# Kernel tuning notes

Hardware: AMD Instinct MI355X
Metric: run time of the kernel (lower is better)

## Reference

```python
import jax, jax.numpy as jnp
import numpy as np

N, D_IN, D_OUT = 10000, 256, 256


def setup_inputs() -> dict:
    key = jax.random.key(0)
    k1, k2, k3, k4 = jax.random.split(key, 4)
    # xavier_uniform with gain=1.414 (as in the torch module)
    def xavier(k, shape, gain=1.414):
        fan_in, fan_out = shape[0], shape[1]
        bound = gain * np.sqrt(6.0 / (fan_in + fan_out))
        return jax.random.uniform(k, shape, jnp.float32, -bound, bound)
    return {
        "input": jax.random.normal(k1, (N, D_IN), jnp.float32),
        "adj": jax.random.randint(k2, (N, N), 0, 2, jnp.int32),  # binary dense adjacency
        "M": N,
        "W": xavier(k3, (D_IN, D_OUT)),
        "b": jnp.zeros((D_OUT,), jnp.float32),
        "a": xavier(k4, (D_OUT, 1)),
    }


def reference(input, adj, M, W, b, a):
    # h = tanh(X W + b); values used for attention logits
    h = jnp.tanh(input @ W + b)          # [N, F]
    inp = input @ W                      # [N, F] (values to aggregate)
    e = (h @ a)[:, 0]                    # [N] per-node logit
    # original also drops neighbors whose h row sums to exactly 0
    valid = (jnp.sum(h, axis=1) != 0)    # [N]
    mask = (adj[:M] > 0) & valid[None, :]  # [M, N]
    neg = jnp.asarray(-1e30, h.dtype)
    scores = jnp.where(mask, e[None, :], neg)           # [M, N]
    m = jnp.max(scores, axis=1, keepdims=True)
    w = jnp.where(mask, jnp.exp(scores - m), 0.0)       # masked exp
    denom = jnp.sum(w, axis=1, keepdims=True)
    att = w / jnp.maximum(denom, 1e-30)  # rows with no neighbors -> all zeros (matches torch zeros init)
    # dropout is identity in eval mode (training=False)
    return att @ inp                     # [M, F]
```

## Files before the change

kernel.cpp:

```cpp
#include <hip/hip_runtime.h>
#include <hip/hip_bf16.h>
#include <cstdint>
#include <cstddef>

#define NN      10000
#define DD      256
#define KSTEPS  313
#define MB256   40
#define KSPLIT  6

typedef __bf16 bf16x8 __attribute__((ext_vector_type(8)));
typedef float  f32x4  __attribute__((ext_vector_type(4)));

#define XG_OFF   0ull
#define XG_SIZE  (32ull * 10000 * 16)
#define WG_OFF   (XG_OFF + XG_SIZE)
#define WG_SIZE  (32ull * 256 * 16)
#define INP_OFF  (WG_OFF + WG_SIZE)
#define INP_SIZE (10000ull * 256 * 4)
#define E_OFF    (INP_OFF + INP_SIZE)
#define E_SIZE   (10016ull * 4)
#define HS_OFF   (E_OFF + E_SIZE)
#define HS_SIZE  (10016ull * 4)
#define G_OFF    (HS_OFF + HS_SIZE)
#define G_SIZE   (10016ull * 4)
#define YG_OFF   (G_OFF + G_SIZE + 256ull)
#define YG_SIZE  (318ull * 1088 * 16)
#define PN_OFF   (YG_OFF + YG_SIZE)
#define PN_SIZE  ((size_t)KSPLIT * 10000 * 272 * 4)

__device__ __forceinline__ void gl_lds16(const void* g, void* lds) {
    __builtin_amdgcn_global_load_lds(
        (const __attribute__((address_space(1))) unsigned int*)g,
        (__attribute__((address_space(3))) unsigned int*)lds,
        16, 0, 0);
}

__global__ __launch_bounds__(256) void k_build_xg(const float* __restrict__ X,
                                                  bf16x8* __restrict__ XG) {
    int idx = blockIdx.x * 256 + threadIdx.x;
    int row = idx >> 5;
    int q   = idx & 31;
    const float* src = X + row * 256 + q * 8;
    bf16x8 v;
#pragma unroll
    for (int j = 0; j < 8; ++j) v[j] = (__bf16)src[j];
    XG[q * 10000 + row] = v;
}

__global__ __launch_bounds__(256) void k_build_wg(const float* __restrict__ W,
                                                  bf16x8* __restrict__ WG) {
    int e = blockIdx.x * 256 + threadIdx.x;
    int q = e >> 8;
    int n = e & 255;
    bf16x8 v;
#pragma unroll
    for (int j = 0; j < 8; ++j) v[j] = (__bf16)W[(q * 8 + j) * 256 + n];
    WG[e] = v;
}

__global__ __launch_bounds__(256) void k_gemm1(const bf16x8* __restrict__ XG,
                                               const bf16x8* __restrict__ WG,
                                               const float* __restrict__ bvec,
                                               const float* __restrict__ avec,
                                               float* __restrict__ inp,
                                               float* __restrict__ evec,
                                               float* __restrict__ hsumv) {
    __shared__ bf16x8 Ash[320];
    __shared__ bf16x8 Bsh[1024];
    __shared__ float ePart[4][80];
    __shared__ float hPart[4][80];
    int tid = threadIdx.x, wid = tid >> 6, lane = tid & 63;
    int l15 = lane & 15, l4 = lane >> 4;
    int mb = blockIdx.x;

    f32x4 acc[4][5];
#pragma unroll
    for (int c = 0; c < 4; ++c)
#pragma unroll
        for (int rt = 0; rt < 5; ++rt) acc[c][rt] = f32x4{0.f, 0.f, 0.f, 0.f};

    for (int kb = 0; kb < 8; ++kb) {
        for (int rr = wid; rr < 5; rr += 4) {
            int c = rr * 64 + lane;
            int g = c / 80, r = c - g * 80;
            gl_lds16(XG + ((kb * 4 + g) * 10000 + mb * 80 + r), (char*)Ash + rr * 1024);
        }
        for (int rr = wid; rr < 16; rr += 4)
            gl_lds16(WG + kb * 1024 + rr * 64 + lane, (char*)Bsh + rr * 1024);
        __syncthreads();

        bf16x8 af[5];
#pragma unroll
        for (int rt = 0; rt < 5; ++rt) af[rt] = Ash[l4 * 80 + rt * 16 + l15];
#pragma unroll
        for (int c = 0; c < 4; ++c) {
            bf16x8 bf = Bsh[l4 * 256 + (wid * 4 + c) * 16 + l15];
#pragma unroll
            for (int rt = 0; rt < 5; ++rt)
                acc[c][rt] = __builtin_amdgcn_mfma_f32_16x16x32_bf16(af[rt], bf, acc[c][rt], 0, 0, 0);
        }
        __syncthreads();
    }

    float pe[5][4], ph[5][4];
#pragma unroll
    for (int rt = 0; rt < 5; ++rt)
#pragma unroll
        for (int rg = 0; rg < 4; ++rg) { pe[rt][rg] = 0.f; ph[rt][rg] = 0.f; }

#pragma unroll
    for (int c = 0; c < 4; ++c) {
        int col = (wid * 4 + c) * 16 + l15;
        float av = avec[col];
        float bv = bvec[col];
#pragma unroll
        for (int rt = 0; rt < 5; ++rt) {
#pragma unroll
            for (int rg = 0; rg < 4; ++rg) {
                int row = mb * 80 + rt * 16 + l4 * 4 + rg;
                float v = acc[c][rt][rg];
                inp[row * 256 + col] = v;
                float h = tanhf(v + bv);
                pe[rt][rg] += h * av;
                ph[rt][rg] += h;
            }
        }
    }
#pragma unroll
    for (int rt = 0; rt < 5; ++rt) {
#pragma unroll
        for (int rg = 0; rg < 4; ++rg) {
            float se = pe[rt][rg], sh = ph[rt][rg];
#pragma unroll
            for (int m = 1; m < 16; m <<= 1) {
                se += __shfl_xor(se, m);
                sh += __shfl_xor(sh, m);
            }
            if (l15 == 0) {
                int lr = rt * 16 + l4 * 4 + rg;
                ePart[wid][lr] = se;
                hPart[wid][lr] = sh;
            }
        }
    }
    __syncthreads();
    if (tid < 80) {
        float e = ePart[0][tid] + ePart[1][tid] + ePart[2][tid] + ePart[3][tid];
        float h = hPart[0][tid] + hPart[1][tid] + hPart[2][tid] + hPart[3][tid];
        evec[mb * 80 + tid] = e;
        hsumv[mb * 80 + tid] = h;
    }
}

__global__ __launch_bounds__(1024) void k_softmax_g(const float* __restrict__ evec,
                                                    const float* __restrict__ hsumv,
                                                    float* __restrict__ gv) {
    __shared__ float red[1024];
    int tid = threadIdx.x;
    float m = -3.0e38f;
    for (int i = tid; i < NN; i += 1024)
        if (hsumv[i] != 0.0f) m = fmaxf(m, evec[i]);
    red[tid] = m;
    __syncthreads();
    for (int s = 512; s > 0; s >>= 1) {
        if (tid < s) red[tid] = fmaxf(red[tid], red[tid + s]);
        __syncthreads();
    }
    float gmax = red[0];
    if (gmax < -1.0e37f) gmax = 0.0f;
    for (int i = tid; i < 10016; i += 1024) {
        float g = 0.0f;
        if (i < NN && hsumv[i] != 0.0f) g = expf(evec[i] - gmax);
        gv[i] = g;
    }
}

__global__ __launch_bounds__(256) void k_build_yg(const float* __restrict__ inp,
                                                  const float* __restrict__ gv,
                                                  bf16x8* __restrict__ YG) {
    int kb = blockIdx.x;
    for (int c = threadIdx.x; c < 1088; c += 256) {
        int gq = c / 272, n = c - gq * 272;
        int k0 = kb * 32 + gq * 8;
        bf16x8 v;
#pragma unroll
        for (int j = 0; j < 8; ++j) {
            int k = k0 + j;
            float val = 0.0f;
            if (k < NN) {
                float gk = gv[k];
                if (n < 256) val = gk * inp[k * 256 + n];
                else if (n == 256) val = gk;
            }
            v[j] = (__bf16)val;
        }
        YG[kb * 1088 + c] = v;
    }
}

__device__ __forceinline__ bf16x8 cvt_adj(int4 a, int4 b) {
    union { bf16x8 v; unsigned int u[4]; } r;
    r.u[0] = (a.x > 0 ? 0x3F80u : 0u) | (a.y > 0 ? 0x3F800000u : 0u);
    r.u[1] = (a.z > 0 ? 0x3F80u : 0u) | (a.w > 0 ? 0x3F800000u : 0u);
    r.u[2] = (b.x > 0 ? 0x3F80u : 0u) | (b.y > 0 ? 0x3F800000u : 0u);
    r.u[3] = (b.z > 0 ? 0x3F80u : 0u) | (b.w > 0 ? 0x3F800000u : 0u);
    return r.v;
}

__global__ __launch_bounds__(1024, 4) void k_attn_gemm(const int* __restrict__ adj,
                                                       const bf16x8* __restrict__ YG,
                                                       float* __restrict__ pnum) {
    __shared__ bf16x8 Bsh[2][1088];
    int tid = threadIdx.x, wid = tid >> 6, lane = tid & 63;
    int l15 = lane & 15, l4 = lane >> 4;

    int phys = blockIdx.x;
    int logical = (phys & 7) * 30 + (phys >> 3);
    int kc = logical / MB256, mb = logical % MB256;
    int s0 = (kc * KSTEPS) / KSPLIT, s1 = ((kc + 1) * KSTEPS) / KSPLIT;

    const int* pR = adj + (size_t)min(mb * 256 + wid * 16 + l15, NN - 1) * 10000;
    int kgrp = l4 * 8;

    f32x4 acc[17];
#pragma unroll
    for (int ct = 0; ct < 17; ++ct) acc[ct] = f32x4{0.f, 0.f, 0.f, 0.f};

    int4 aA[2];

    auto stageB = [&](int sTile, int bufIdx) {
        const bf16x8* src = YG + (size_t)sTile * 1088;
        char* dst = (char*)&Bsh[bufIdx][0];
        gl_lds16(src + wid * 64 + lane, dst + wid * 1024);
        if (wid == 0) gl_lds16(src + 1024 + lane, dst + 16384);
    };
    auto loadA = [&](int sTile) {
        int kk = min(sTile * 32 + kgrp, 9992);
        const int4* p = (const int4*)(pR + kk);
        aA[0] = p[0]; aA[1] = p[1];
    };
    auto compute = [&](bf16x8 fa, int bufIdx) {
#pragma unroll
        for (int ct = 0; ct < 17; ++ct) {
            bf16x8 fb = Bsh[bufIdx][l4 * 272 + ct * 16 + l15];
            acc[ct] = __builtin_amdgcn_mfma_f32_16x16x32_bf16(fa, fb, acc[ct], 0, 0, 0);
        }
    };

    stageB(s0, 0);
    __builtin_amdgcn_sched_barrier(0);
    loadA(s0);
    asm volatile("s_waitcnt vmcnt(2)" ::: "memory");
    __builtin_amdgcn_s_barrier();

    int buf = 0;
    for (int s = s0; s < s1 - 1; ++s) {
        stageB(s + 1, buf ^ 1);
        __builtin_amdgcn_sched_barrier(0);
        bf16x8 fa = cvt_adj(aA[0], aA[1]);
        loadA(s + 1);
        __builtin_amdgcn_sched_barrier(0);
        compute(fa, buf);
        asm volatile("s_waitcnt vmcnt(2)" ::: "memory");
        __builtin_amdgcn_s_barrier();
        buf ^= 1;
    }
    {
        bf16x8 fa = cvt_adj(aA[0], aA[1]);
        compute(fa, buf);
    }

    float* base = pnum + (size_t)kc * 10000 * 272;
    int r0 = mb * 256 + wid * 16;
#pragma unroll
    for (int ct = 0; ct < 17; ++ct) {
        int col = ct * 16 + l15;
#pragma unroll
        for (int rg = 0; rg < 4; ++rg) {
            int row = r0 + l4 * 4 + rg;
            if (row < NN) base[(size_t)row * 272 + col] = acc[ct][rg];
        }
    }
}

__global__ __launch_bounds__(256) void k_finalize(const float* __restrict__ pnum,
                                                  float* __restrict__ out) {
    int idx = blockIdx.x * 256 + threadIdx.x;
    int i = idx >> 6, q = idx & 63;
    float4 sv = {0.f, 0.f, 0.f, 0.f};
    float den = 0.f;
#pragma unroll
    for (int kc = 0; kc < KSPLIT; ++kc) {
        const float* row = pnum + ((size_t)kc * 10000 + i) * 272;
        float4 v = ((const float4*)row)[q];
        sv.x += v.x; sv.y += v.y; sv.z += v.z; sv.w += v.w;
        den += row[256];
    }
    float r = 1.0f / fmaxf(den, 1e-30f);
    float4 o;
    o.x = sv.x * r; o.y = sv.y * r; o.z = sv.z * r; o.w = sv.w * r;
    ((float4*)(out + (size_t)i * 256))[q] = o;
}

extern "C" void kernel_launch(void* const* d_in, const int* in_sizes, int n_in,
                              void* d_out, int out_size, void* d_ws, size_t ws_size,
                              hipStream_t stream) {
    const float* X    = (const float*)d_in[0];
    const int*   adj  = (const int*)d_in[1];
    const float* W    = (const float*)d_in[3];
    const float* bvec = (const float*)d_in[4];
    const float* avec = (const float*)d_in[5];
    float* out = (float*)d_out;

    char* ws = (char*)d_ws;
    bf16x8* XG   = (bf16x8*)(ws + XG_OFF);
    bf16x8* WG   = (bf16x8*)(ws + WG_OFF);
    float*  inp  = (float*)(ws + INP_OFF);
    float*  evec = (float*)(ws + E_OFF);
    float*  hsv  = (float*)(ws + HS_OFF);
    float*  gv   = (float*)(ws + G_OFF);
    bf16x8* YG   = (bf16x8*)(ws + YG_OFF);
    float*  pnum = (float*)(ws + PN_OFF);

    k_build_xg<<<1250, 256, 0, stream>>>(X, XG);
    k_build_wg<<<32, 256, 0, stream>>>(W, WG);
    k_gemm1<<<125, 256, 0, stream>>>(XG, WG, bvec, avec, inp, evec, hsv);
    k_softmax_g<<<1, 1024, 0, stream>>>(evec, hsv, gv);
    k_build_yg<<<318, 256, 0, stream>>>(inp, gv, YG);
    k_attn_gemm<<<MB256 * KSPLIT, 1024, 0, stream>>>(adj, YG, pnum);
    k_finalize<<<2500, 256, 0, stream>>>(pnum, out);
}
```

Measured before the change: 192.0 us.

## Give each wave two row tiles and triple-buffer B with batched adjacency loads

The attention GEMM now runs 512-thread blocks in which each wave computes two 16-row tiles, so every B fragment read from LDS feeds two MFMAs. Adjacency loads are batched four k-steps ahead into 16 int4 registers, and the B tile uses a three-deep LDS ring so loads stay further ahead of compute. YG is padded to 320 tiles to cover the deeper prefetch. The aim is less LDS traffic per MFMA and better hiding of the bandwidth-bound adj stream, at the cost of much higher register pressure (34 accumulators plus 16 prefetch registers) and fewer waves per block.

```diff
diff --git a/kernel.cpp b/kernel.cpp
--- a/kernel.cpp
+++ b/kernel.cpp
@@ -25,7 +25,7 @@
 #define G_OFF    (HS_OFF + HS_SIZE)
 #define G_SIZE   (10016ull * 4)
 #define YG_OFF   (G_OFF + G_SIZE + 256ull)
-#define YG_SIZE  (318ull * 1088 * 16)
+#define YG_SIZE  (320ull * 1088 * 16)
 #define PN_OFF   (YG_OFF + YG_SIZE)
 #define PN_SIZE  ((size_t)KSPLIT * 10000 * 272 * 4)
 
@@ -208,10 +208,10 @@
     return r.v;
 }
 
-__global__ __launch_bounds__(1024, 4) void k_attn_gemm(const int* __restrict__ adj,
-                                                       const bf16x8* __restrict__ YG,
-                                                       float* __restrict__ pnum) {
-    __shared__ bf16x8 Bsh[2][1088];
+__global__ __launch_bounds__(512, 2) void k_attn_gemm(const int* __restrict__ adj,
+                                                      const bf16x8* __restrict__ YG,
+                                                      float* __restrict__ pnum) {
+    __shared__ bf16x8 Bsh[3][1088];
     int tid = threadIdx.x, wid = tid >> 6, lane = tid & 63;
     int l15 = lane & 15, l4 = lane >> 4;
 
@@ -220,66 +220,117 @@
     int kc = logical / MB256, mb = logical % MB256;
     int s0 = (kc * KSTEPS) / KSPLIT, s1 = ((kc + 1) * KSTEPS) / KSPLIT;
 
-    const int* pR = adj + (size_t)min(mb * 256 + wid * 16 + l15, NN - 1) * 10000;
+    int r0w = mb * 256 + wid * 32;
+    const int* pA = adj + (size_t)min(r0w + l15, NN - 1) * 10000;
+    const int* pB = adj + (size_t)min(r0w + 16 + l15, NN - 1) * 10000;
     int kgrp = l4 * 8;
 
-    f32x4 acc[17];
-#pragma unroll
-    for (int ct = 0; ct < 17; ++ct) acc[ct] = f32x4{0.f, 0.f, 0.f, 0.f};
-
-    int4 aA[2];
+    f32x4 acc[2][17];
+#pragma unroll
+    for (int t = 0; t < 2; ++t)
+#pragma unroll
+        for (int ct = 0; ct < 17; ++ct) acc[t][ct] = f32x4{0.f, 0.f, 0.f, 0.f};
+
+    int4 aA[16];
 
     auto stageB = [&](int sTile, int bufIdx) {
         const bf16x8* src = YG + (size_t)sTile * 1088;
         char* dst = (char*)&Bsh[bufIdx][0];
-        gl_lds16(src + wid * 64 + lane, dst + wid * 1024);
-        if (wid == 0) gl_lds16(src + 1024 + lane, dst + 16384);
+        gl_lds16(src + (2 * wid) * 64 + lane, dst + (2 * wid) * 1024);
+        gl_lds16(src + (2 * wid + 1) * 64 + lane, dst + (2 * wid + 1) * 1024);
+        gl_lds16(src + 16 * 64 + lane, dst + 16 * 1024);
     };
-    auto loadA = [&](int sTile) {
-        int kk = min(sTile * 32 + kgrp, 9992);
-        const int4* p = (const int4*)(pR + kk);
-        aA[0] = p[0]; aA[1] = p[1];
+    auto loadBatch = [&](int S) {
+#pragma unroll
+        for (int j = 0; j < 4; ++j) {
+            int kk = min((S + j) * 32 + kgrp, 9992);
+            const int4* p0 = (const int4*)(pA + kk);
+            const int4* p1 = (const int4*)(pB + kk);
+            aA[j * 4 + 0] = p0[0]; aA[j * 4 + 1] = p0[1];
+            aA[j * 4 + 2] = p1[0]; aA[j * 4 + 3] = p1[1];
+        }
     };
-    auto compute = [&](bf16x8 fa, int bufIdx) {
+    auto compute = [&](bf16x8 fa0, bf16x8 fa1, int b) {
 #pragma unroll
         for (int ct = 0; ct < 17; ++ct) {
-            bf16x8 fb = Bsh[bufIdx][l4 * 272 + ct * 16 + l15];
-            acc[ct] = __builtin_amdgcn_mfma_f32_16x16x32_bf16(fa, fb, acc[ct], 0, 0, 0);
+            bf16x8 fb = Bsh[b][l4 * 272 + ct * 16 + l15];
+            acc[0][ct] = __builtin_amdgcn_mfma_f32_16x16x32_bf16(fa0, fb, acc[0][ct], 0, 0, 0);
+            acc[1][ct] = __builtin_amdgcn_mfma_f32_16x16x32_bf16(fa1, fb, acc[1][ct], 0, 0, 0);
         }
     };
 
-    stageB(s0, 0);
+    loadBatch(s0);
+    int b0 = s0 % 3;
+    int b1 = b0 + 1; if (b1 > 2) b1 -= 3;
+    int b2 = b1 + 1; if (b2 > 2) b2 -= 3;
+    stageB(s0, b0);
+    stageB(s0 + 1, b1);
     __builtin_amdgcn_sched_barrier(0);
-    loadA(s0);
-    asm volatile("s_waitcnt vmcnt(2)" ::: "memory");
+    asm volatile("s_waitcnt vmcnt(3)" ::: "memory");
     __builtin_amdgcn_s_barrier();
 
-    int buf = 0;
-    for (int s = s0; s < s1 - 1; ++s) {
-        stageB(s + 1, buf ^ 1);
-        __builtin_amdgcn_sched_barrier(0);
-        bf16x8 fa = cvt_adj(aA[0], aA[1]);
-        loadA(s + 1);
-        __builtin_amdgcn_sched_barrier(0);
-        compute(fa, buf);
-        asm volatile("s_waitcnt vmcnt(2)" ::: "memory");
-        __builtin_amdgcn_s_barrier();
-        buf ^= 1;
-    }
-    {
-        bf16x8 fa = cvt_adj(aA[0], aA[1]);
-        compute(fa, buf);
+    int G = s0;
+    while (G + 4 <= s1) {
+        {
+            stageB(G + 2, b2);
+            __builtin_amdgcn_sched_barrier(0);
+            bf16x8 fa0 = cvt_adj(aA[0], aA[1]);
+            bf16x8 fa1 = cvt_adj(aA[2], aA[3]);
+            compute(fa0, fa1, b0);
+            asm volatile("s_waitcnt vmcnt(3)" ::: "memory");
+            __builtin_amdgcn_s_barrier();
+        }
+        {
+            stageB(G + 3, b0);
+            __builtin_amdgcn_sched_barrier(0);
+            bf16x8 fa0 = cvt_adj(aA[4], aA[5]);
+            bf16x8 fa1 = cvt_adj(aA[6], aA[7]);
+            compute(fa0, fa1, b1);
+            asm volatile("s_waitcnt vmcnt(3)" ::: "memory");
+            __builtin_amdgcn_s_barrier();
+        }
+        {
+            stageB(G + 4, b1);
+            __builtin_amdgcn_sched_barrier(0);
+            bf16x8 fa0 = cvt_adj(aA[8], aA[9]);
+            bf16x8 fa1 = cvt_adj(aA[10], aA[11]);
+            compute(fa0, fa1, b2);
+            asm volatile("s_waitcnt vmcnt(3)" ::: "memory");
+            __builtin_amdgcn_s_barrier();
+        }
+        {
+            stageB(G + 5, b2);
+            __builtin_amdgcn_sched_barrier(0);
+            bf16x8 fa0 = cvt_adj(aA[12], aA[13]);
+            bf16x8 fa1 = cvt_adj(aA[14], aA[15]);
+            loadBatch(G + 4);
+            __builtin_amdgcn_sched_barrier(0);
+            compute(fa0, fa1, b0);
+            asm volatile("s_waitcnt vmcnt(19)" ::: "memory");
+            __builtin_amdgcn_s_barrier();
+        }
+        G += 4;
+        b0 = b0 + 1; if (b0 > 2) b0 -= 3;
+        b1 = b0 + 1; if (b1 > 2) b1 -= 3;
+        b2 = b1 + 1; if (b2 > 2) b2 -= 3;
+    }
+    if (G < s1) {
+        bf16x8 fa0 = cvt_adj(aA[0], aA[1]);
+        bf16x8 fa1 = cvt_adj(aA[2], aA[3]);
+        compute(fa0, fa1, b0);
     }
 
     float* base = pnum + (size_t)kc * 10000 * 272;
-    int r0 = mb * 256 + wid * 16;
-#pragma unroll
-    for (int ct = 0; ct < 17; ++ct) {
-        int col = ct * 16 + l15;
-#pragma unroll
-        for (int rg = 0; rg < 4; ++rg) {
-            int row = r0 + l4 * 4 + rg;
-            if (row < NN) base[(size_t)row * 272 + col] = acc[ct][rg];
+#pragma unroll
+    for (int t = 0; t < 2; ++t) {
+#pragma unroll
+        for (int ct = 0; ct < 17; ++ct) {
+            int col = ct * 16 + l15;
+#pragma unroll
+            for (int rg = 0; rg < 4; ++rg) {
+                int row = r0w + t * 16 + l4 * 4 + rg;
+                if (row < NN) base[(size_t)row * 272 + col] = acc[t][ct][rg];
+            }
         }
     }
 }
@@ -327,7 +378,7 @@
     k_build_wg<<<32, 256, 0, stream>>>(W, WG);
     k_gemm1<<<125, 256, 0, stream>>>(XG, WG, bvec, avec, inp, evec, hsv);
     k_softmax_g<<<1, 1024, 0, stream>>>(evec, hsv, gv);
-    k_build_yg<<<318, 256, 0, stream>>>(inp, gv, YG);
-    k_attn_gemm<<<MB256 * KSPLIT, 1024, 0, stream>>>(adj, YG, pnum);
+    k_build_yg<<<320, 256, 0, stream>>>(inp, gv, YG);
+    k_attn_gemm<<<MB256 * KSPLIT, 512, 0, stream>>>(adj, YG, pnum);
     k_finalize<<<2500, 256, 0, stream>>>(pnum, out);
 }
```

After: 203.9 us. 6.2% more time.
